# Kernel tuning notes

Hardware: AMD Instinct MI355X
Metric: run time of the kernel (lower is better)

Reference implementation:

```python
import jax, jax.numpy as jnp
import numpy as np

H = 4  # heads_n (sequential refinement heads)


def _layer_norm(x, g, b, eps=1e-5):
    mu = jnp.mean(x, axis=-1, keepdims=True)
    var = jnp.mean((x - mu) ** 2, axis=-1, keepdims=True)
    return (x - mu) * jax.lax.rsqrt(var + eps) * g + b


def _pose_enc(S, F):
    # Faithful translation of PoseEncoding._make_pe_buffer
    pos = jnp.arange(S, dtype=jnp.float32)[:, None]            # (S,1)
    div = (1.0 / (1000.0 ** (2.0 * jnp.arange(F, dtype=jnp.float32) / F)))[None, :]  # (1,F)
    pe = jnp.zeros((S, F), jnp.float32)
    pe = pe.at[0::2, :].set(jnp.sin(pos[0::2] * div))
    pe = pe.at[1::2, :].set(jnp.cos(pos[1::2] * div))
    return pe  # (S,F)


def setup_inputs() -> dict:
    key = jax.random.key(0)
    ks = jax.random.split(key, 6)
    B, S, C = 4, 2048, 1024
    std = 0.02
    return {
        "x": jax.random.normal(ks[0], (B, S, C), jnp.float32),
        "fc_in_w": jax.random.normal(ks[1], (C, C), jnp.float32) * std,
        "fc_in_b": jnp.zeros((C,), jnp.float32),
        "ln_g": jnp.ones((C,), jnp.float32),
        "ln_b": jnp.zeros((C,), jnp.float32),
        "qkv_w": jax.random.normal(ks[2], (H, 3 * C, C), jnp.float32) * std,
        "qkv_b": jnp.zeros((H, 3 * C), jnp.float32),
        "proj_w": jax.random.normal(ks[3], (H, C, C), jnp.float32) * std,
        "proj_b": jnp.zeros((H, C), jnp.float32),
        "fc_out_w": jax.random.normal(ks[4], (C, C), jnp.float32) * std,
        "fc_out_b": jnp.zeros((C,), jnp.float32),
    }


def reference(x, fc_in_w, fc_in_b, ln_g, ln_b, qkv_w, qkv_b, proj_w, proj_b, fc_out_w, fc_out_b):
    B, S, C = x.shape
    gelu = lambda t: jax.nn.gelu(t, approximate=False)  # nn.GELU default = exact erf
    h = x @ fc_in_w.T + fc_in_b                         # fc_in
    h = _layer_norm(h, ln_g, ln_b)
    pred = None
    for i in range(qkv_w.shape[0]):                     # sequential heads loop (eval mode: dropout = identity)
        qkv = gelu(h @ qkv_w[i].T + qkv_b[i])           # (B,S,3C)
        qkv = qkv.reshape(B, S, 3, C)
        q, k, v = qkv[:, :, 0], qkv[:, :, 1], qkv[:, :, 2]
        scores = jnp.einsum('bsc,btc->bst', q, k) * (1.0 / C)  # (B,S,S), mask is None
        att = jnp.einsum('bst,btc->bsc', scores, v)     # matmul BEFORE softmax (non-standard order)
        att = jax.nn.softmax(att, axis=-1)
        h = gelu(att @ proj_w[i].T + proj_b[i])
        if pred is None:
            pred = h
        else:
            h = h + pred                                 # residual with first head's output
    out = h @ fc_out_w.T + fc_out_b
    return out + _pose_enc(S, out.shape[-1])[None]      # PoseEncoding add
```

## Files before the change

### kernel.cpp

```cpp
#include <hip/hip_runtime.h>
#include <math.h>

typedef unsigned short u16;
typedef __bf16 bf16x8 __attribute__((ext_vector_type(8)));
typedef float f32x4  __attribute__((ext_vector_type(4)));
typedef float f32x16 __attribute__((ext_vector_type(16)));
typedef u16   u16x4  __attribute__((ext_vector_type(4)));

#define GPTR(p) ((__attribute__((address_space(1))) void*)(p))
#define LPTR(p) ((__attribute__((address_space(3))) void*)(p))

__device__ __forceinline__ float bf2f(u16 h) { return __uint_as_float(((unsigned)h) << 16); }
__device__ __forceinline__ u16 f2bf(float f) {
    unsigned u = __float_as_uint(f);
    return (u16)((u + 0x7fffu + ((u >> 16) & 1u)) >> 16);
}
__device__ __forceinline__ float gelu_f(float x) {
    float u = 0.7978845608f * x * (1.0f + 0.044715f * x * x);
    float e = __expf(2.0f * u);
    float t = 1.0f - 2.0f / (e + 1.0f);
    return 0.5f * x * (1.0f + t);
}

template<int MODE>
__global__ __launch_bounds__(256, 4)
void gemm_bt(const u16* __restrict__ A, int lda, long sA,
             const u16* __restrict__ B, int ldb, long sB,
             void* __restrict__ Cout, int ldc, long sC,
             const float* __restrict__ bias,
             const u16* __restrict__ addend,
             int K, float scale)
{
    __shared__ u16 lds[16384];
    u16* lA = lds;
    u16* lB = lds + 8192;
    const int t    = threadIdx.x;
    const int lane = t & 63;
    const int wid  = t >> 6;
    const int wm   = (wid & 1) * 64;
    const int wn   = (wid >> 1) * 64;
    const int m32  = lane & 31;
    const int h    = lane >> 5;
    const int bz   = blockIdx.z;

    const long rowA0 = (long)blockIdx.y * 128;
    const long colB0 = (long)blockIdx.x * 128;
    const u16* Ab = A + (long)bz * sA + rowA0 * lda;
    const u16* Bb = B + (long)bz * sB + colB0 * ldb;

    const int rt  = t >> 3;
    const int kcg = ((t & 7) ^ (rt & 7)) * 8;
    const u16* gA[4]; const u16* gB[4];
    #pragma unroll
    for (int j = 0; j < 4; j++) {
        gA[j] = Ab + (long)(j * 32 + rt) * lda + kcg;
        gB[j] = Bb + (long)(j * 32 + rt) * ldb + kcg;
    }
    u16* dA = lA + t * 8;
    u16* dB = lB + t * 8;

    f32x16 acc[2][2];
    #pragma unroll
    for (int i = 0; i < 2; i++)
        #pragma unroll
        for (int j = 0; j < 2; j++)
            #pragma unroll
            for (int r = 0; r < 16; r++) acc[i][j][r] = 0.f;

    const int sg = m32 & 7;
    const u16* fA[4]; const u16* fB[4];
    #pragma unroll
    for (int kh = 0; kh < 4; kh++) {
        fA[kh] = lA + (wm + m32) * 64 + 8 * ((kh * 2 + h) ^ sg);
        fB[kh] = lB + (wn + m32) * 64 + 8 * ((kh * 2 + h) ^ sg);
    }

    for (int k0 = 0; k0 < K; k0 += 64) {
        #pragma unroll
        for (int j = 0; j < 4; j++) {
            __builtin_amdgcn_global_load_lds(GPTR(gA[j] + k0), LPTR(dA + j * 2048), 16, 0, 0);
            __builtin_amdgcn_global_load_lds(GPTR(gB[j] + k0), LPTR(dB + j * 2048), 16, 0, 0);
        }
        __syncthreads();
        #pragma unroll
        for (int kh = 0; kh < 4; kh++) {
            bf16x8 a0 = *(const bf16x8*)(fA[kh]);
            bf16x8 a1 = *(const bf16x8*)(fA[kh] + 2048);
            bf16x8 b0 = *(const bf16x8*)(fB[kh]);
            bf16x8 b1 = *(const bf16x8*)(fB[kh] + 2048);
            acc[0][0] = __builtin_amdgcn_mfma_f32_32x32x16_bf16(a0, b0, acc[0][0], 0, 0, 0);
            acc[0][1] = __builtin_amdgcn_mfma_f32_32x32x16_bf16(a0, b1, acc[0][1], 0, 0, 0);
            acc[1][0] = __builtin_amdgcn_mfma_f32_32x32x16_bf16(a1, b0, acc[1][0], 0, 0, 0);
            acc[1][1] = __builtin_amdgcn_mfma_f32_32x32x16_bf16(a1, b1, acc[1][1], 0, 0, 0);
        }
        __syncthreads();
    }

    float* Cf = (float*)Cout + (long)bz * sC;
    u16*   Cu = (u16*)Cout + (long)bz * sC;
    float* sw_ = (float*)lds + wid * 1024;
    const long rb = rowA0 + wm;
    const long cb = colB0 + wn;
    const int prow = lane >> 3;
    const int c4   = (lane & 7) * 4;
    #pragma unroll
    for (int mi = 0; mi < 2; mi++) {
        #pragma unroll
        for (int ni = 0; ni < 2; ni++) {
            #pragma unroll
            for (int r = 0; r < 16; r++)
                sw_[((r & 3) + 8 * (r >> 2) + 4 * h) * 32 + m32] = acc[mi][ni][r];
            #pragma unroll
            for (int p = 0; p < 4; p++) {
                const int  row  = p * 8 + prow;
                const long grow = rb + mi * 32 + row;
                const long gcol = cb + ni * 32 + c4;
                f32x4 v = *(const f32x4*)&sw_[row * 32 + c4];
                float4 bvv = {0.f, 0.f, 0.f, 0.f};
                if constexpr (MODE >= 2) bvv = *(const float4*)&bias[gcol];
                if constexpr (MODE == 1) {
                    #pragma unroll
                    for (int e = 0; e < 4; e++) v[e] *= scale;
                }
                v[0] += bvv.x; v[1] += bvv.y; v[2] += bvv.z; v[3] += bvv.w;
                if constexpr (MODE == 3 || MODE == 4) {
                    #pragma unroll
                    for (int e = 0; e < 4; e++) v[e] = gelu_f(v[e]);
                }
                if constexpr (MODE == 4) {
                    u16x4 ad = *(const u16x4*)&addend[grow * (long)ldc + gcol];
                    #pragma unroll
                    for (int e = 0; e < 4; e++) v[e] += bf2f(ad[e]);
                }
                if constexpr (MODE == 5) {
                    *(f32x4*)&Cf[grow * (long)ldc + gcol] = v;
                } else {
                    u16x4 o = { f2bf(v[0]), f2bf(v[1]), f2bf(v[2]), f2bf(v[3]) };
                    *(u16x4*)&Cu[grow * (long)ldc + gcol] = o;
                }
            }
        }
    }
}

__global__ __launch_bounds__(256)
void cvt_all(const float* __restrict__ s0, u16* __restrict__ d0, long n0,
             const float* __restrict__ s1, u16* __restrict__ d1, long n1,
             const float* __restrict__ s2, u16* __restrict__ d2, long n2,
             const float* __restrict__ s3, u16* __restrict__ d3, long n3,
             const float* __restrict__ s4, u16* __restrict__ d4, long n4)
{
    long i = ((long)blockIdx.x * 256 + threadIdx.x) * 4;
    const float* s; u16* d;
    if      (i < n0)                    { s = s0;  d = d0; }
    else if ((i -= n0) < n1)            { s = s1;  d = d1; }
    else if ((i -= n1) < n2)            { s = s2;  d = d2; }
    else if ((i -= n2) < n3)            { s = s3;  d = d3; }
    else if ((i -= n3) < n4)            { s = s4;  d = d4; }
    else return;
    float4 v = *(const float4*)(s + i);
    u16x4 o = { f2bf(v.x), f2bf(v.y), f2bf(v.z), f2bf(v.w) };
    *(u16x4*)(d + i) = o;
}

__global__ __launch_bounds__(256)
void ln_kernel(const u16* __restrict__ in, u16* __restrict__ out,
               const float* __restrict__ g, const float* __restrict__ b)
{
    const int row = blockIdx.x;
    const int t = threadIdx.x;
    const u16* r = in + (long)row * 1024;
    float x[4];
    float s = 0.f, s2 = 0.f;
    #pragma unroll
    for (int j = 0; j < 4; j++) { x[j] = bf2f(r[t + 256 * j]); s += x[j]; s2 += x[j] * x[j]; }
    __shared__ float sm[8];
    const int lane = t & 63, wid = t >> 6;
    #pragma unroll
    for (int o = 32; o > 0; o >>= 1) { s += __shfl_down(s, o, 64); s2 += __shfl_down(s2, o, 64); }
    if (lane == 0) { sm[wid] = s; sm[4 + wid] = s2; }
    __syncthreads();
    s  = sm[0] + sm[1] + sm[2] + sm[3];
    s2 = sm[4] + sm[5] + sm[6] + sm[7];
    const float mean = s * (1.f / 1024.f);
    const float var  = s2 * (1.f / 1024.f) - mean * mean;
    const float rstd = rsqrtf(var + 1e-5f);
    u16* o = out + (long)row * 1024;
    #pragma unroll
    for (int j = 0; j < 4; j++) {
        int c = t + 256 * j;
        o[c] = f2bf((x[j] - mean) * rstd * g[c] + b[c]);
    }
}

__global__ __launch_bounds__(256)
void softmax_kernel(u16* __restrict__ io)
{
    const int row = blockIdx.x;
    const int t = threadIdx.x;
    u16* r = io + (long)row * 1024;
    float x[4];
    float m = -1e30f;
    #pragma unroll
    for (int j = 0; j < 4; j++) { x[j] = bf2f(r[t + 256 * j]); m = fmaxf(m, x[j]); }
    __shared__ float sm[8];
    const int lane = t & 63, wid = t >> 6;
    #pragma unroll
    for (int o = 32; o > 0; o >>= 1) m = fmaxf(m, __shfl_down(m, o, 64));
    if (lane == 0) sm[wid] = m;
    __syncthreads();
    m = fmaxf(fmaxf(sm[0], sm[1]), fmaxf(sm[2], sm[3]));
    float e[4];
    float s = 0.f;
    #pragma unroll
    for (int j = 0; j < 4; j++) { e[j] = __expf(x[j] - m); s += e[j]; }
    #pragma unroll
    for (int o = 32; o > 0; o >>= 1) s += __shfl_down(s, o, 64);
    if (lane == 0) sm[4 + wid] = s;
    __syncthreads();
    s = sm[4] + sm[5] + sm[6] + sm[7];
    const float inv = 1.f / s;
    #pragma unroll
    for (int j = 0; j < 4; j++) r[t + 256 * j] = f2bf(e[j] * inv);
}

__global__ void transpose_v(const u16* __restrict__ qkv, u16* __restrict__ vT)
{
    __shared__ u16 tile[32][33];
    const int b  = blockIdx.z;
    const int t0 = blockIdx.x * 32;
    const int c0 = blockIdx.y * 32;
    const int tx = threadIdx.x, ty = threadIdx.y;
    #pragma unroll
    for (int i = ty; i < 32; i += 8)
        tile[i][tx] = qkv[((long)(b * 2048 + t0 + i)) * 3072 + 2048 + c0 + tx];
    __syncthreads();
    #pragma unroll
    for (int i = ty; i < 32; i += 8)
        vT[((long)(b * 1024 + c0 + i)) * 2048 + t0 + tx] = tile[tx][i];
}

__global__ __launch_bounds__(256)
void add_pe(float* __restrict__ out)
{
    long i = (long)blockIdx.x * 256 + threadIdx.x;
    const int f = (int)(i & 1023);
    const int s = (int)((i >> 10) & 2047);
    const float div = __expf(-(float)f * 0.013491709529261986f);
    const float arg = (float)s * div;
    const float pe = (s & 1) ? cosf(arg) : sinf(arg);
    out[i] += pe;
}

extern "C" void kernel_launch(void* const* d_in, const int* in_sizes, int n_in,
                              void* d_out, int out_size, void* d_ws, size_t ws_size,
                              hipStream_t stream)
{
    const float* x        = (const float*)d_in[0];
    const float* fc_in_w  = (const float*)d_in[1];
    const float* fc_in_b  = (const float*)d_in[2];
    const float* ln_g     = (const float*)d_in[3];
    const float* ln_b     = (const float*)d_in[4];
    const float* qkv_w    = (const float*)d_in[5];
    const float* qkv_b    = (const float*)d_in[6];
    const float* proj_w   = (const float*)d_in[7];
    const float* proj_b   = (const float*)d_in[8];
    const float* fc_out_w = (const float*)d_in[9];
    const float* fc_out_b = (const float*)d_in[10];

    char* w = (char*)d_ws;
    size_t off = 0;
    auto carve = [&](size_t bytes) -> void* {
        void* p = w + off;
        off += (bytes + 255) & ~(size_t)255;
        return p;
    };
    u16* xb   = (u16*)carve(16777216);
    u16* hY   = xb;
    u16* wfci = (u16*)carve(2097152);
    u16* wqkv = (u16*)carve(25165824);
    u16* wprj = (u16*)carve(8388608);
    u16* wfco = (u16*)carve(2097152);
    u16* t0   = (u16*)carve(50331648);
    u16* att  = t0;
    u16* hX   = (u16*)carve(16777216);
    u16* pred = (u16*)carve(16777216);
    u16* vT   = (u16*)carve(16777216);
    u16* sc   = (u16*)carve(33554432);

    cvt_all<<<dim3(26624), dim3(256), 0, stream>>>(
        x, xb, 8388608L, fc_in_w, wfci, 1048576L, qkv_w, wqkv, 12582912L,
        proj_w, wprj, 4194304L, fc_out_w, wfco, 1048576L);

    gemm_bt<2><<<dim3(8, 64, 1), 256, 0, stream>>>(xb, 1024, 0, wfci, 1024, 0,
                                                   t0, 1024, 0, fc_in_b, nullptr, 1024, 1.0f);
    ln_kernel<<<8192, 256, 0, stream>>>(t0, hX, ln_g, ln_b);

    const u16* hin[4] = { hX, pred, hX, hY };
    u16* hout[4]      = { pred, hX, hY, hX };

    for (int i = 0; i < 4; i++) {
        gemm_bt<3><<<dim3(24, 64, 1), 256, 0, stream>>>(hin[i], 1024, 0,
            wqkv + (long)i * 3145728, 1024, 0, t0, 3072, 0,
            qkv_b + (long)i * 3072, nullptr, 1024, 1.0f);
        transpose_v<<<dim3(64, 32, 4), dim3(32, 8), 0, stream>>>(t0, vT);
        gemm_bt<1><<<dim3(16, 16, 4), 256, 0, stream>>>(t0, 3072, 6291456,
            t0 + 1024, 3072, 6291456, sc, 2048, 4194304,
            nullptr, nullptr, 1024, 1.0f / 1024.0f);
        gemm_bt<0><<<dim3(8, 16, 4), 256, 0, stream>>>(sc, 2048, 4194304,
            vT, 2048, 2097152, att, 1024, 2097152,
            nullptr, nullptr, 2048, 1.0f);
        softmax_kernel<<<8192, 256, 0, stream>>>(att);
        if (i == 0)
            gemm_bt<3><<<dim3(8, 64, 1), 256, 0, stream>>>(att, 1024, 0,
                wprj, 1024, 0, hout[0], 1024, 0, proj_b, nullptr, 1024, 1.0f);
        else
            gemm_bt<4><<<dim3(8, 64, 1), 256, 0, stream>>>(att, 1024, 0,
                wprj + (long)i * 1048576, 1024, 0, hout[i], 1024, 0,
                proj_b + (long)i * 1024, pred, 1024, 1.0f);
    }

    gemm_bt<5><<<dim3(8, 64, 1), 256, 0, stream>>>(hX, 1024, 0, wfco, 1024, 0,
                                                   d_out, 1024, 0, fc_out_b, nullptr, 1024, 1.0f);
    add_pe<<<32768, 256, 0, stream>>>((float*)d_out);
}
```

Measured before the change: 1.070 ms.

## Pre-swizzle weights into MFMA fragment layout and load B directly from global

Weight matrices are converted to bf16 in a tiled layout that matches the MFMA B-operand fragment order. The weight-side GEMMs can then load B fragments straight from global memory into registers, skipping the LDS staging. This halves LDS usage per block and removes LDS reads for B. The cost is more global traffic, since B is no longer shared across waves through LDS and each wave loads its own fragments. It also adds register pressure and a separate weight-conversion kernel.

```diff
diff --git a/kernel.cpp b/kernel.cpp
--- a/kernel.cpp
+++ b/kernel.cpp
@@ -6,6 +6,7 @@
 typedef float f32x4  __attribute__((ext_vector_type(4)));
 typedef float f32x16 __attribute__((ext_vector_type(16)));
 typedef u16   u16x4  __attribute__((ext_vector_type(4)));
+typedef u16   u16x8  __attribute__((ext_vector_type(8)));
 
 #define GPTR(p) ((__attribute__((address_space(1))) void*)(p))
 #define LPTR(p) ((__attribute__((address_space(3))) void*)(p))
@@ -22,7 +23,7 @@
     return 0.5f * x * (1.0f + t);
 }
 
-template<int MODE>
+template<int MODE, int BG>
 __global__ __launch_bounds__(256, 4)
 void gemm_bt(const u16* __restrict__ A, int lda, long sA,
              const u16* __restrict__ B, int ldb, long sB,
@@ -31,7 +32,7 @@
              const u16* __restrict__ addend,
              int K, float scale)
 {
-    __shared__ u16 lds[16384];
+    __shared__ u16 lds[BG ? 8192 : 16384];
     u16* lA = lds;
     u16* lB = lds + 8192;
     const int t    = threadIdx.x;
@@ -46,18 +47,25 @@
     const long rowA0 = (long)blockIdx.y * 128;
     const long colB0 = (long)blockIdx.x * 128;
     const u16* Ab = A + (long)bz * sA + rowA0 * lda;
-    const u16* Bb = B + (long)bz * sB + colB0 * ldb;
 
     const int rt  = t >> 3;
     const int kcg = ((t & 7) ^ (rt & 7)) * 8;
-    const u16* gA[4]; const u16* gB[4];
-    #pragma unroll
-    for (int j = 0; j < 4; j++) {
-        gA[j] = Ab + (long)(j * 32 + rt) * lda + kcg;
-        gB[j] = Bb + (long)(j * 32 + rt) * ldb + kcg;
-    }
+    const u16* gA[4];
+    #pragma unroll
+    for (int j = 0; j < 4; j++) gA[j] = Ab + (long)(j * 32 + rt) * lda + kcg;
     u16* dA = lA + t * 8;
-    u16* dB = lB + t * 8;
+
+    const u16* gB[4]; u16* dB = lB + t * 8;
+    const u16* gb0 = nullptr; const u16* gb1 = nullptr;
+    if constexpr (BG) {
+        const int nt0 = (int)((colB0 + wn) >> 5);
+        gb0 = B + (long)nt0 * (K >> 4) * 512 + lane * 8;
+        gb1 = gb0 + (long)(K >> 4) * 512;
+    } else {
+        const u16* Bb = B + (long)bz * sB + colB0 * ldb;
+        #pragma unroll
+        for (int j = 0; j < 4; j++) gB[j] = Bb + (long)(j * 32 + rt) * ldb + kcg;
+    }
 
     f32x16 acc[2][2];
     #pragma unroll
@@ -72,22 +80,36 @@
     #pragma unroll
     for (int kh = 0; kh < 4; kh++) {
         fA[kh] = lA + (wm + m32) * 64 + 8 * ((kh * 2 + h) ^ sg);
-        fB[kh] = lB + (wn + m32) * 64 + 8 * ((kh * 2 + h) ^ sg);
+        if constexpr (!BG) fB[kh] = lB + (wn + m32) * 64 + 8 * ((kh * 2 + h) ^ sg);
     }
 
     for (int k0 = 0; k0 < K; k0 += 64) {
         #pragma unroll
-        for (int j = 0; j < 4; j++) {
+        for (int j = 0; j < 4; j++)
             __builtin_amdgcn_global_load_lds(GPTR(gA[j] + k0), LPTR(dA + j * 2048), 16, 0, 0);
-            __builtin_amdgcn_global_load_lds(GPTR(gB[j] + k0), LPTR(dB + j * 2048), 16, 0, 0);
+        bf16x8 bg[2][4];
+        if constexpr (BG) {
+            #pragma unroll
+            for (int kh = 0; kh < 4; kh++) {
+                bg[0][kh] = *(const bf16x8*)(gb0 + (long)k0 * 32 + kh * 512);
+                bg[1][kh] = *(const bf16x8*)(gb1 + (long)k0 * 32 + kh * 512);
+            }
+        } else {
+            #pragma unroll
+            for (int j = 0; j < 4; j++)
+                __builtin_amdgcn_global_load_lds(GPTR(gB[j] + k0), LPTR(dB + j * 2048), 16, 0, 0);
         }
         __syncthreads();
         #pragma unroll
         for (int kh = 0; kh < 4; kh++) {
             bf16x8 a0 = *(const bf16x8*)(fA[kh]);
             bf16x8 a1 = *(const bf16x8*)(fA[kh] + 2048);
-            bf16x8 b0 = *(const bf16x8*)(fB[kh]);
-            bf16x8 b1 = *(const bf16x8*)(fB[kh] + 2048);
+            bf16x8 b0, b1;
+            if constexpr (BG) { b0 = bg[0][kh]; b1 = bg[1][kh]; }
+            else {
+                b0 = *(const bf16x8*)(fB[kh]);
+                b1 = *(const bf16x8*)(fB[kh] + 2048);
+            }
             acc[0][0] = __builtin_amdgcn_mfma_f32_32x32x16_bf16(a0, b0, acc[0][0], 0, 0, 0);
             acc[0][1] = __builtin_amdgcn_mfma_f32_32x32x16_bf16(a0, b1, acc[0][1], 0, 0, 0);
             acc[1][0] = __builtin_amdgcn_mfma_f32_32x32x16_bf16(a1, b0, acc[1][0], 0, 0, 0);
@@ -144,23 +166,43 @@
 }
 
 __global__ __launch_bounds__(256)
-void cvt_all(const float* __restrict__ s0, u16* __restrict__ d0, long n0,
-             const float* __restrict__ s1, u16* __restrict__ d1, long n1,
-             const float* __restrict__ s2, u16* __restrict__ d2, long n2,
-             const float* __restrict__ s3, u16* __restrict__ d3, long n3,
-             const float* __restrict__ s4, u16* __restrict__ d4, long n4)
+void cvt_x(const float* __restrict__ in, u16* __restrict__ out, long n)
 {
     long i = ((long)blockIdx.x * 256 + threadIdx.x) * 4;
-    const float* s; u16* d;
-    if      (i < n0)                    { s = s0;  d = d0; }
-    else if ((i -= n0) < n1)            { s = s1;  d = d1; }
-    else if ((i -= n1) < n2)            { s = s2;  d = d2; }
-    else if ((i -= n2) < n3)            { s = s3;  d = d3; }
-    else if ((i -= n3) < n4)            { s = s4;  d = d4; }
-    else return;
-    float4 v = *(const float4*)(s + i);
-    u16x4 o = { f2bf(v.x), f2bf(v.y), f2bf(v.z), f2bf(v.w) };
-    *(u16x4*)(d + i) = o;
+    if (i < n) {
+        float4 v = *(const float4*)(in + i);
+        u16x4 o = { f2bf(v.x), f2bf(v.y), f2bf(v.z), f2bf(v.w) };
+        *(u16x4*)(out + i) = o;
+    }
+}
+
+__global__ __launch_bounds__(256)
+void cvt_wg(const float* __restrict__ qkvw, u16* __restrict__ dqkv,
+            const float* __restrict__ projw, u16* __restrict__ dproj,
+            const float* __restrict__ fciw, u16* __restrict__ dfci,
+            const float* __restrict__ fcow, u16* __restrict__ dfco)
+{
+    __shared__ u16 sl[2048];
+    const int nt = blockIdx.y;
+    const int ks = blockIdx.x;
+    const int t  = threadIdx.x;
+    const float* src; u16* dst; int nl;
+    if      (nt < 384) { src = qkvw;  dst = dqkv;  nl = nt; }
+    else if (nt < 512) { src = projw; dst = dproj; nl = nt - 384; }
+    else if (nt < 544) { src = fciw;  dst = dfci;  nl = nt - 512; }
+    else               { src = fcow;  dst = dfco;  nl = nt - 544; }
+    const int n32 = t >> 3;
+    const int kq  = t & 7;
+    const float* s = src + ((long)nl * 32 + n32) * 1024 + ks * 64 + kq * 8;
+    float4 v0 = *(const float4*)s;
+    float4 v1 = *(const float4*)(s + 4);
+    u16x8 o = { f2bf(v0.x), f2bf(v0.y), f2bf(v0.z), f2bf(v0.w),
+                f2bf(v1.x), f2bf(v1.y), f2bf(v1.z), f2bf(v1.w) };
+    const int slot = (kq >> 1) * 64 + (kq & 1) * 32 + n32;
+    *(u16x8*)&sl[slot * 8] = o;
+    __syncthreads();
+    u16* d = dst + (long)nl * 32768 + ks * 2048 + t * 8;
+    *(u16x8*)d = *(const u16x8*)&sl[t * 8];
 }
 
 __global__ __launch_bounds__(256)
@@ -288,39 +330,39 @@
     u16* vT   = (u16*)carve(16777216);
     u16* sc   = (u16*)carve(33554432);
 
-    cvt_all<<<dim3(26624), dim3(256), 0, stream>>>(
-        x, xb, 8388608L, fc_in_w, wfci, 1048576L, qkv_w, wqkv, 12582912L,
-        proj_w, wprj, 4194304L, fc_out_w, wfco, 1048576L);
-
-    gemm_bt<2><<<dim3(8, 64, 1), 256, 0, stream>>>(xb, 1024, 0, wfci, 1024, 0,
-                                                   t0, 1024, 0, fc_in_b, nullptr, 1024, 1.0f);
+    cvt_x<<<dim3(8192), dim3(256), 0, stream>>>(x, xb, 8388608L);
+    cvt_wg<<<dim3(16, 576), dim3(256), 0, stream>>>(qkv_w, wqkv, proj_w, wprj,
+                                                    fc_in_w, wfci, fc_out_w, wfco);
+
+    gemm_bt<2,1><<<dim3(8, 64, 1), 256, 0, stream>>>(xb, 1024, 0, wfci, 0, 0,
+                                                     t0, 1024, 0, fc_in_b, nullptr, 1024, 1.0f);
     ln_kernel<<<8192, 256, 0, stream>>>(t0, hX, ln_g, ln_b);
 
     const u16* hin[4] = { hX, pred, hX, hY };
     u16* hout[4]      = { pred, hX, hY, hX };
 
     for (int i = 0; i < 4; i++) {
-        gemm_bt<3><<<dim3(24, 64, 1), 256, 0, stream>>>(hin[i], 1024, 0,
-            wqkv + (long)i * 3145728, 1024, 0, t0, 3072, 0,
+        gemm_bt<3,1><<<dim3(24, 64, 1), 256, 0, stream>>>(hin[i], 1024, 0,
+            wqkv + (long)i * 3145728, 0, 0, t0, 3072, 0,
             qkv_b + (long)i * 3072, nullptr, 1024, 1.0f);
         transpose_v<<<dim3(64, 32, 4), dim3(32, 8), 0, stream>>>(t0, vT);
-        gemm_bt<1><<<dim3(16, 16, 4), 256, 0, stream>>>(t0, 3072, 6291456,
+        gemm_bt<1,0><<<dim3(16, 16, 4), 256, 0, stream>>>(t0, 3072, 6291456,
             t0 + 1024, 3072, 6291456, sc, 2048, 4194304,
             nullptr, nullptr, 1024, 1.0f / 1024.0f);
-        gemm_bt<0><<<dim3(8, 16, 4), 256, 0, stream>>>(sc, 2048, 4194304,
+        gemm_bt<0,0><<<dim3(8, 16, 4), 256, 0, stream>>>(sc, 2048, 4194304,
             vT, 2048, 2097152, att, 1024, 2097152,
             nullptr, nullptr, 2048, 1.0f);
         softmax_kernel<<<8192, 256, 0, stream>>>(att);
         if (i == 0)
-            gemm_bt<3><<<dim3(8, 64, 1), 256, 0, stream>>>(att, 1024, 0,
-                wprj, 1024, 0, hout[0], 1024, 0, proj_b, nullptr, 1024, 1.0f);
+            gemm_bt<3,1><<<dim3(8, 64, 1), 256, 0, stream>>>(att, 1024, 0,
+                wprj, 0, 0, hout[0], 1024, 0, proj_b, nullptr, 1024, 1.0f);
         else
-            gemm_bt<4><<<dim3(8, 64, 1), 256, 0, stream>>>(att, 1024, 0,
-                wprj + (long)i * 1048576, 1024, 0, hout[i], 1024, 0,
+            gemm_bt<4,1><<<dim3(8, 64, 1), 256, 0, stream>>>(att, 1024, 0,
+                wprj + (long)i * 1048576, 0, 0, hout[i], 1024, 0,
                 proj_b + (long)i * 1024, pred, 1024, 1.0f);
     }
 
-    gemm_bt<5><<<dim3(8, 64, 1), 256, 0, stream>>>(hX, 1024, 0, wfco, 1024, 0,
-                                                   d_out, 1024, 0, fc_out_b, nullptr, 1024, 1.0f);
+    gemm_bt<5,1><<<dim3(8, 64, 1), 256, 0, stream>>>(hX, 1024, 0, wfco, 0, 0,
+                                                     d_out, 1024, 0, fc_out_b, nullptr, 1024, 1.0f);
     add_pe<<<32768, 256, 0, stream>>>((float*)d_out);
 }
```

New measurement: 1.047 ms. -2.1%, faster.
